# Optimization experiments

Measured on AMD Instinct MI355X. Metric: run time of the kernel, lower is better.

Reference implementation:

```python
import jax, jax.numpy as jnp
import numpy as np

DIM = 768
HEADS = 12
HEAD_DIM = DIM // HEADS
SCALE = HEAD_DIM ** (-0.5)
BATCH = 1
SEQ = 4096


def setup_inputs() -> dict:
    key = jax.random.key(0)
    ks = jax.random.split(key, 5)
    x = jax.random.normal(ks[0], (BATCH, SEQ, DIM), dtype=jnp.float32)
    # Linear params stored (in, out) for y = x @ W + b
    w_qkv = jax.random.normal(ks[1], (DIM, 3 * DIM), dtype=jnp.float32) * (DIM ** -0.5)
    b_qkv = jnp.zeros((3 * DIM,), dtype=jnp.float32)
    w_proj = jax.random.normal(ks[2], (DIM, DIM), dtype=jnp.float32) * (DIM ** -0.5)
    b_proj = jnp.zeros((DIM,), dtype=jnp.float32)
    return {"x": x, "w_qkv": w_qkv, "b_qkv": b_qkv, "w_proj": w_proj, "b_proj": b_proj}


def reference(x, w_qkv, b_qkv, w_proj, b_proj):
    B, S, _ = x.shape
    qkv = x @ w_qkv + b_qkv                              # [B,S,3*DIM]
    qkv = qkv.reshape(B, S, 3, HEADS, HEAD_DIM)
    q, k, v = qkv[:, :, 0], qkv[:, :, 1], qkv[:, :, 2]   # [B,S,H,D]
    # scaled dot-product attention, full score matrix as in the original
    attn = jnp.einsum("bqhd,bkhd->bhqk", q * SCALE, k)   # [B,H,S,S]
    attn = jax.nn.softmax(attn, axis=-1)
    out = jnp.einsum("bhqk,bkhd->bqhd", attn, v)         # [B,S,H,D]
    out = out.reshape(B, S, DIM)
    return out @ w_proj + b_proj
```

## Files before the change

### kernel.cpp

```cpp
#include <hip/hip_runtime.h>
#include <hip/hip_bf16.h>

#define SEQ   4096
#define DIM   768
#define HEADS 12
#define NQKV  2304
#define QSCALE 0.18033688011f

#if __has_builtin(__builtin_amdgcn_exp2f)
#define EXP2(x) __builtin_amdgcn_exp2f(x)
#else
#define EXP2(x) __expf((x) * 0.69314718056f)
#endif

typedef __bf16 bf16_t;
typedef bf16_t bf16x8 __attribute__((ext_vector_type(8)));
typedef float  f32x4  __attribute__((ext_vector_type(4)));
typedef float  f32x16 __attribute__((ext_vector_type(16)));
typedef unsigned short u16;
typedef unsigned int   u32;

static __device__ __forceinline__ float bf2f(u16 v) {
    union { float f; unsigned u; } x; x.u = ((unsigned)v) << 16; return x.f;
}
static __device__ __forceinline__ u16 f2bf(float f) {
    union { float f; unsigned u; } x; x.f = f;
    unsigned r = x.u + 0x7fff + ((x.u >> 16) & 1);
    return (u16)(r >> 16);
}
static __device__ __forceinline__ u32 fbits(float f) {
    union { float f; unsigned u; } x; x.f = f; return x.u;
}
static __device__ __forceinline__ void gload_lds16(const u16* g, u16* l) {
    __builtin_amdgcn_global_load_lds(
        (const __attribute__((address_space(1))) unsigned int*)g,
        (__attribute__((address_space(3))) unsigned int*)l, 16, 0, 0);
}

static __device__ __forceinline__ int detect_f32(const u32* __restrict__ x) {
    int lane = threadIdx.x & 63;
    int cnt = 0;
#pragma unroll
    for (int i = 0; i < 8; ++i) {
        u32 w = x[lane * 8 + i];
        cnt += (((w >> 7) & 0xFF) >= 0x8F) ? 1 : 0;
    }
#pragma unroll
    for (int m = 1; m < 64; m <<= 1) cnt += __shfl_xor(cnt, m);
    return cnt >= 64;
}

__global__ __launch_bounds__(256) void prep(
    const void* __restrict__ x, const void* __restrict__ wqkv,
    const void* __restrict__ bqkv, const void* __restrict__ wproj,
    const void* __restrict__ bproj,
    u16* __restrict__ cvt, u16* __restrict__ wqkvT, u16* __restrict__ wprojT)
{
    __shared__ u16 tile[64][65];
    const bool f32 = detect_f32((const u32*)x) != 0;
    const int b = blockIdx.x;
    const int t = threadIdx.x;

    if (b < 576) {
        const void* src; u16* dst; int K, N, tx, ty;
        if (b < 432) { src = wqkv; dst = wqkvT; K = DIM; N = NQKV; tx = b % 36; ty = b / 36; }
        else { int bb = b - 432; src = wproj; dst = wprojT; K = DIM; N = DIM; tx = bb % 12; ty = bb / 12; }
        const int k0 = ty * 64, n0 = tx * 64;
#pragma unroll
        for (int i = 0; i < 16; ++i) {
            int idx = i * 256 + t;
            int r = idx >> 6, c = idx & 63;
            size_t si = (size_t)(k0 + r) * N + n0 + c;
            tile[r][c] = f32 ? f2bf(((const float*)src)[si]) : ((const u16*)src)[si];
        }
        __syncthreads();
#pragma unroll
        for (int i = 0; i < 16; ++i) {
            int idx = i * 256 + t;
            int r = idx >> 6, c = idx & 63;
            dst[(size_t)(n0 + r) * K + k0 + c] = tile[c][r];
        }
    } else {
        const int SX = SEQ * DIM, e1 = SX + NQKV;
        const int n_cvt = e1 + DIM;
        for (int i = (b - 576) * 256 + t; i < n_cvt; i += 200 * 256) {
            const void* s; int off;
            if      (i < SX) { s = x; off = i; }
            else if (i < e1) { s = bqkv; off = i - SX; }
            else             { s = bproj; off = i - e1; }
            cvt[i] = f32 ? f2bf(((const float*)s)[off]) : ((const u16*)s)[off];
        }
    }
}

template<int MODE>
__global__ __launch_bounds__(256) void gemm128(
    const u16* __restrict__ A, const u16* __restrict__ BT, const u16* __restrict__ bias,
    u16* __restrict__ C0, float* __restrict__ Cf, u16* __restrict__ VT,
    const u32* __restrict__ xdet, int M, int N, int K)
{
    __shared__ union SharedLds {
        struct { u16 a[3][128 * 32]; u16 b[3][128 * 32]; } s;
        u16 t[128 * 136];
    } lds;

    const int t    = threadIdx.x;
    const int w    = t >> 6;
    const int lane = t & 63;
    const int l15  = lane & 15;
    const int quad = lane >> 4;
    const int wm   = w >> 1, wn = w & 1;
    const int m0   = blockIdx.y * 128, n0 = blockIdx.x * 128;

    const int srow = w * 32 + (lane >> 2);
    const int kch  = (lane & 3) * 8;
    const u16* asrc = A  + (size_t)(m0 + srow) * K + kch;
    const u16* bsrc = BT + (size_t)(n0 + srow) * K + kch;
    const int wst = w * 32 * 32;

    f32x4 acc[4][4] = {};

    u16 *aA = lds.s.a[0], *aB = lds.s.a[1], *aC = lds.s.a[2];
    u16 *bA = lds.s.b[0], *bB = lds.s.b[1], *bC = lds.s.b[2];

    auto STAGE = [&](u16* ad, u16* bd) {
        gload_lds16(asrc,          ad + wst);
        gload_lds16(asrc + 16 * K, ad + wst + 16 * 32);
        gload_lds16(bsrc,          bd + wst);
        gload_lds16(bsrc + 16 * K, bd + wst + 16 * 32);
        asrc += 32; bsrc += 32;
    };
    auto COMPUTE = [&](const u16* ab_, const u16* bb_) {
        const u16* ab = ab_ + (wm * 64 + l15) * 32 + quad * 8;
        const u16* bb = bb_ + (wn * 64 + l15) * 32 + quad * 8;
        bf16x8 af[4], bfr[4];
#pragma unroll
        for (int i = 0; i < 4; ++i) af[i]  = *(const bf16x8*)(ab + i * 16 * 32);
#pragma unroll
        for (int j = 0; j < 4; ++j) bfr[j] = *(const bf16x8*)(bb + j * 16 * 32);
#pragma unroll
        for (int i = 0; i < 4; ++i)
#pragma unroll
            for (int j = 0; j < 4; ++j)
                acc[i][j] = __builtin_amdgcn_mfma_f32_16x16x32_bf16(af[i], bfr[j], acc[i][j], 0, 0, 0);
    };

    const int NK = K >> 5;
    STAGE(aA, bA);
    STAGE(aB, bB);
    for (int kt = 0; kt < NK - 2; ++kt) {
        asm volatile("s_waitcnt vmcnt(4)" ::: "memory");
        __builtin_amdgcn_s_barrier();
        STAGE(aC, bC);
        COMPUTE(aA, bA);
        { u16* tt = aA; aA = aB; aB = aC; aC = tt; }
        { u16* tt = bA; bA = bB; bB = bC; bC = tt; }
    }
    asm volatile("s_waitcnt vmcnt(4)" ::: "memory");
    __builtin_amdgcn_s_barrier();
    COMPUTE(aA, bA);
    { u16* tt = aA; aA = aB; aB = aC; aC = tt; }
    { u16* tt = bA; bA = bB; bB = bC; bC = tt; }
    asm volatile("s_waitcnt vmcnt(0)" ::: "memory");
    __builtin_amdgcn_s_barrier();
    COMPUTE(aA, bA);

    if constexpr (MODE == 1) {
        if (n0 >= 1536) {
            __syncthreads();
#pragma unroll
            for (int i = 0; i < 4; ++i)
#pragma unroll
                for (int j = 0; j < 4; ++j)
#pragma unroll
                    for (int r = 0; r < 4; ++r) {
                        int ml = wm * 64 + i * 16 + quad * 4 + r;
                        int nl = wn * 64 + j * 16 + l15;
                        int mpl = (ml & ~15) | (ml & 3) |
                                  (((ml >> 2) & 1) << 3) | (((ml >> 3) & 1) << 2);
                        float v = acc[i][j][r] + bf2f(bias[n0 + nl]);
                        lds.t[nl * 136 + mpl] = f2bf(v);
                    }
            __syncthreads();
            const int rr = t >> 4;
            const int mo = (t & 15) * 8;
#pragma unroll
            for (int it = 0; it < 8; ++it) {
                int nl = rr + it * 16;
                *(bf16x8*)(VT + (size_t)(n0 - 1536 + nl) * SEQ + m0 + mo) =
                    *(const bf16x8*)(lds.t + nl * 136 + mo);
            }
            return;
        }
    }

    bool outf32 = false;
    if (MODE == 0) outf32 = detect_f32(xdet) != 0;
#pragma unroll
    for (int i = 0; i < 4; ++i)
#pragma unroll
        for (int j = 0; j < 4; ++j)
#pragma unroll
            for (int r = 0; r < 4; ++r) {
                int m = m0 + wm * 64 + i * 16 + quad * 4 + r;
                int n = n0 + wn * 64 + j * 16 + l15;
                float v = acc[i][j][r] + bf2f(bias[n]);
                if (MODE == 0) {
                    if (outf32) Cf[(size_t)m * N + n] = v;
                    else        C0[(size_t)m * N + n] = f2bf(v);
                } else {
                    float s = (n < 768) ? v * QSCALE : v;
                    C0[(size_t)m * 1536 + n] = f2bf(s);
                }
            }
}

__global__ __launch_bounds__(256, 3) void attn_kernel(
    const u16* __restrict__ qk, const u16* __restrict__ vt, u16* __restrict__ out)
{
    __shared__ u16 k_lds[3][64 * 64];
    __shared__ u16 v_lds[3][64 * 64];
    __shared__ float l_red[2][2][32];

    const int t    = threadIdx.x;
    const int w    = t >> 6;
    const int lane = t & 63;
    const int l31  = lane & 31;
    const int h    = lane >> 5;
    const int wq   = w & 1;
    const int wk   = w >> 1;

    const int lin     = blockIdx.x + (blockIdx.y << 6);
    const int logical = (lin & 7) * 96 + (lin >> 3);
    const int head    = logical >> 6;
    const int q0      = (logical & 63) * 64 + wq * 32;

    const u16* qrow = qk + (size_t)(q0 + l31) * 1536 + head * 64 + h * 8;
    bf16x8 qb[4];
#pragma unroll
    for (int s = 0; s < 4; ++s) qb[s] = *(const bf16x8*)(qrow + 16 * s);

    bf16x8 ones;
#pragma unroll
    for (int j = 0; j < 8; ++j) ones[j] = (bf16_t)1.0f;

    const f32x16 fz = {};

    const int srow = 8 * w + (lane >> 3);
    const int cs   = ((lane & 7) - srow) & 7;
    const u16* kst0 = qk + 768 + head * 64 + (size_t)srow * 1536 + cs * 8;
    const u16* kst1 = kst0 + (size_t)32 * 1536;
    const u16* vst0 = vt + (size_t)head * 64 * SEQ + (size_t)srow * SEQ + cs * 8;
    const u16* vst1 = vst0 + (size_t)32 * SEQ;
    const int woff = 8 * w * 64;

    const int krow = 32 * wk + l31;

    f32x16 o0 = {}, o1 = {}, lac = {};

    auto SK = [&](u16* kd) {
        gload_lds16(kst0, kd + woff);
        gload_lds16(kst1, kd + woff + 32 * 64);
        kst0 += (size_t)64 * 1536;
        kst1 += (size_t)64 * 1536;
    };
    auto SV = [&](u16* vd) {
        gload_lds16(vst0, vd + woff);
        gload_lds16(vst1, vd + woff + 32 * 64);
        vst0 += 64;
        vst1 += 64;
    };

    auto QK = [&](const u16* kb) -> f32x16 {
        const u16* kbase = kb + krow * 64;
        bf16x8 ka0 = *(const bf16x8*)(kbase + (((0 + h + krow) & 7) * 8));
        bf16x8 ka1 = *(const bf16x8*)(kbase + (((2 + h + krow) & 7) * 8));
        bf16x8 ka2 = *(const bf16x8*)(kbase + (((4 + h + krow) & 7) * 8));
        bf16x8 ka3 = *(const bf16x8*)(kbase + (((6 + h + krow) & 7) * 8));
        __builtin_amdgcn_s_setprio(1);
        f32x16 st = __builtin_amdgcn_mfma_f32_32x32x16_bf16(ka0, qb[0], fz, 0, 0, 0);
        st = __builtin_amdgcn_mfma_f32_32x32x16_bf16(ka1, qb[1], st, 0, 0, 0);
        st = __builtin_amdgcn_mfma_f32_32x32x16_bf16(ka2, qb[2], st, 0, 0, 0);
        st = __builtin_amdgcn_mfma_f32_32x32x16_bf16(ka3, qb[3], st, 0, 0, 0);
        __builtin_amdgcn_s_setprio(0);
        return st;
    };

    auto SMPV = [&](const f32x16& st, const u16* vb) {
        u32 q32[8];
#pragma unroll
        for (int i = 0; i < 8; ++i) {
            float pe = EXP2(st[2 * i]);
            float po = EXP2(st[2 * i + 1]);
            q32[i] = __builtin_amdgcn_perm(fbits(po), fbits(pe), 0x07060302u);
        }
        union { u32 u[4]; bf16x8 v; } pf0, pf1;
#pragma unroll
        for (int i = 0; i < 4; ++i) { pf0.u[i] = q32[i]; pf1.u[i] = q32[4 + i]; }
        __builtin_amdgcn_s_setprio(1);
#pragma unroll
        for (int s2 = 0; s2 < 2; ++s2) {
            const int c = 4 * wk + 2 * s2 + h;
            bf16x8 vb0 = *(const bf16x8*)(vb + l31 * 64 + (((c + l31) & 7) * 8));
            bf16x8 vb1 = *(const bf16x8*)(vb + (32 + l31) * 64 + (((c + 32 + l31) & 7) * 8));
            const bf16x8 pv = s2 ? pf1.v : pf0.v;
            o0  = __builtin_amdgcn_mfma_f32_32x32x16_bf16(pv, vb0, o0, 0, 0, 0);
            o1  = __builtin_amdgcn_mfma_f32_32x32x16_bf16(pv, vb1, o1, 0, 0, 0);
            lac = __builtin_amdgcn_mfma_f32_32x32x16_bf16(pv, ones, lac, 0, 0, 0);
        }
        __builtin_amdgcn_s_setprio(0);
    };

    u16 *kA = &k_lds[0][0], *kB = &k_lds[1][0], *kC = &k_lds[2][0];
    u16 *vA = &v_lds[0][0], *vB = &v_lds[1][0], *vC = &v_lds[2][0];

    SK(kA);
    SV(vA);
    SK(kB);
    asm volatile("s_waitcnt vmcnt(4)" ::: "memory");
    __builtin_amdgcn_s_barrier();
    f32x16 stA = QK(kA);
    SV(vB);
    f32x16 stB;

    for (int i = 0; i < 31; ++i) {
        SK(kC);
        asm volatile("s_waitcnt vmcnt(4)" ::: "memory");
        __builtin_amdgcn_s_barrier();
        stB = QK(kB);
        SMPV(stA, vA);
        SV(vC);
        { u16* tt = kA; kA = kB; kB = kC; kC = tt; }
        { u16* tt = vA; vA = vB; vB = vC; vC = tt; }
        SK(kC);
        asm volatile("s_waitcnt vmcnt(4)" ::: "memory");
        __builtin_amdgcn_s_barrier();
        stA = QK(kB);
        SMPV(stB, vA);
        SV(vC);
        { u16* tt = kA; kA = kB; kB = kC; kC = tt; }
        { u16* tt = vA; vA = vB; vB = vC; vC = tt; }
    }
    asm volatile("s_waitcnt vmcnt(2)" ::: "memory");
    __builtin_amdgcn_s_barrier();
    stB = QK(kB);
    SMPV(stA, vA);
    { u16* tt = kA; kA = kB; kB = kC; kC = tt; }
    { u16* tt = vA; vA = vB; vB = vC; vC = tt; }
    asm volatile("s_waitcnt vmcnt(0)" ::: "memory");
    __builtin_amdgcn_s_barrier();
    SMPV(stB, vA);
    __syncthreads();

    if (l31 == 0) {
#pragma unroll
        for (int r = 0; r < 16; ++r) {
            int row = (r & 3) + 8 * (r >> 2) + 4 * h;
            l_red[wq][wk][row] = lac[r];
        }
    }
    float* scr = (wq == 0) ? (float*)&k_lds[0][0] : (float*)&v_lds[0][0];
    if (wk == 1) {
#pragma unroll
        for (int r = 0; r < 16; ++r) {
            int row = (r & 3) + 8 * (r >> 2) + 4 * h;
            scr[row * 64 + l31]      = o0[r];
            scr[row * 64 + 32 + l31] = o1[r];
        }
    }
    __syncthreads();
    if (wk == 0) {
#pragma unroll
        for (int r = 0; r < 16; ++r) {
            int row = (r & 3) + 8 * (r >> 2) + 4 * h;
            float lt   = l_red[wq][0][row] + l_red[wq][1][row];
            float invl = 1.0f / lt;
            float s0 = o0[r] + scr[row * 64 + l31];
            float s1 = o1[r] + scr[row * 64 + 32 + l31];
            size_t gr = (size_t)(q0 + row) * 768 + head * 64;
            out[gr + l31]      = f2bf(s0 * invl);
            out[gr + 32 + l31] = f2bf(s1 * invl);
        }
    }
}

extern "C" void kernel_launch(void* const* d_in, const int* in_sizes, int n_in,
                              void* d_out, int out_size, void* d_ws, size_t ws_size,
                              hipStream_t stream) {
    const int SX = SEQ * DIM;

    u16* base   = (u16*)d_ws;
    u16* xb     = base;
    u16* bqkvb  = xb + SX;
    u16* bprojb = bqkvb + NQKV;
    u16* wqkvT  = bprojb + DIM;
    u16* wprojT = wqkvT + (size_t)NQKV * DIM;
    u16* qkb    = wprojT + (size_t)DIM * DIM;
    u16* vtb    = qkb + (size_t)SEQ * 1536;
    u16* attnb  = xb;

    prep<<<776, 256, 0, stream>>>(
        d_in[0], d_in[1], d_in[2], d_in[3], d_in[4], base, wqkvT, wprojT);
    gemm128<1><<<dim3(NQKV / 128, SEQ / 128), 256, 0, stream>>>(
        xb, wqkvT, bqkvb, qkb, nullptr, vtb, (const u32*)d_in[0],
        SEQ, NQKV, DIM);
    attn_kernel<<<dim3(SEQ / 64, HEADS), 256, 0, stream>>>(qkb, vtb, attnb);
    gemm128<0><<<dim3(DIM / 128, SEQ / 128), 256, 0, stream>>>(
        attnb, wprojT, bprojb, (u16*)d_out, (float*)d_out, nullptr,
        (const u32*)d_in[0], SEQ, DIM, DIM);
}
```

Before: 206.1 us.

## Cut attention V buffers to two for higher occupancy; swizzle GEMM block order

The attention kernel drops from triple to double buffering for V tiles and reuses V LDS for the row-sum reduction. This cuts LDS per block so four blocks can fit per CU instead of three. The V load is now issued after each barrier, which shortens the prefetch distance and may expose load latency. The GEMM also remaps block indices so that consecutive blocks are spread in groups of eight, aiming at better cache locality across XCDs.

```diff
diff --git a/kernel.cpp b/kernel.cpp
--- a/kernel.cpp
+++ b/kernel.cpp
@@ -110,7 +110,12 @@
     const int l15  = lane & 15;
     const int quad = lane >> 4;
     const int wm   = w >> 1, wn = w & 1;
-    const int m0   = blockIdx.y * 128, n0 = blockIdx.x * 128;
+
+    const int lin     = blockIdx.y * gridDim.x + blockIdx.x;
+    const int cpx     = (gridDim.x * gridDim.y) >> 3;
+    const int logical = (lin & 7) * cpx + (lin >> 3);
+    const int m0 = (logical / gridDim.x) * 128;
+    const int n0 = (logical % gridDim.x) * 128;
 
     const int srow = w * 32 + (lane >> 2);
     const int kch  = (lane & 3) * 8;
@@ -215,12 +220,11 @@
             }
 }
 
-__global__ __launch_bounds__(256, 3) void attn_kernel(
+__global__ __launch_bounds__(256, 4) void attn_kernel(
     const u16* __restrict__ qk, const u16* __restrict__ vt, u16* __restrict__ out)
 {
     __shared__ u16 k_lds[3][64 * 64];
-    __shared__ u16 v_lds[3][64 * 64];
-    __shared__ float l_red[2][2][32];
+    __shared__ u16 v_lds[2][64 * 64];
 
     const int t    = threadIdx.x;
     const int w    = t >> 6;
@@ -312,54 +316,52 @@
     };
 
     u16 *kA = &k_lds[0][0], *kB = &k_lds[1][0], *kC = &k_lds[2][0];
-    u16 *vA = &v_lds[0][0], *vB = &v_lds[1][0], *vC = &v_lds[2][0];
+    u16 *v0 = &v_lds[0][0], *v1 = &v_lds[1][0];
 
     SK(kA);
-    SV(vA);
     SK(kB);
+    SV(v0);
     asm volatile("s_waitcnt vmcnt(4)" ::: "memory");
     __builtin_amdgcn_s_barrier();
     f32x16 stA = QK(kA);
-    SV(vB);
     f32x16 stB;
 
     for (int i = 0; i < 31; ++i) {
         SK(kC);
-        asm volatile("s_waitcnt vmcnt(4)" ::: "memory");
+        asm volatile("s_waitcnt vmcnt(2)" ::: "memory");
         __builtin_amdgcn_s_barrier();
+        SV(v1);
         stB = QK(kB);
-        SMPV(stA, vA);
-        SV(vC);
+        SMPV(stA, v0);
         { u16* tt = kA; kA = kB; kB = kC; kC = tt; }
-        { u16* tt = vA; vA = vB; vB = vC; vC = tt; }
         SK(kC);
-        asm volatile("s_waitcnt vmcnt(4)" ::: "memory");
+        asm volatile("s_waitcnt vmcnt(2)" ::: "memory");
         __builtin_amdgcn_s_barrier();
+        SV(v0);
         stA = QK(kB);
-        SMPV(stB, vA);
-        SV(vC);
+        SMPV(stB, v1);
         { u16* tt = kA; kA = kB; kB = kC; kC = tt; }
-        { u16* tt = vA; vA = vB; vB = vC; vC = tt; }
-    }
-    asm volatile("s_waitcnt vmcnt(2)" ::: "memory");
-    __builtin_amdgcn_s_barrier();
-    stB = QK(kB);
-    SMPV(stA, vA);
-    { u16* tt = kA; kA = kB; kB = kC; kC = tt; }
-    { u16* tt = vA; vA = vB; vB = vC; vC = tt; }
+    }
     asm volatile("s_waitcnt vmcnt(0)" ::: "memory");
     __builtin_amdgcn_s_barrier();
-    SMPV(stB, vA);
+    SV(v1);
+    stB = QK(kB);
+    SMPV(stA, v0);
+    { u16* tt = kA; kA = kB; kB = kC; kC = tt; }
+    asm volatile("s_waitcnt vmcnt(0)" ::: "memory");
+    __builtin_amdgcn_s_barrier();
+    SMPV(stB, v1);
     __syncthreads();
 
+    float* lred = (float*)&v_lds[1][0];
     if (l31 == 0) {
 #pragma unroll
         for (int r = 0; r < 16; ++r) {
             int row = (r & 3) + 8 * (r >> 2) + 4 * h;
-            l_red[wq][wk][row] = lac[r];
-        }
-    }
-    float* scr = (wq == 0) ? (float*)&k_lds[0][0] : (float*)&v_lds[0][0];
+            lred[(wq * 2 + wk) * 32 + row] = lac[r];
+        }
+    }
+    float* scr = (wq == 0) ? (float*)&k_lds[0][0] : (float*)&k_lds[1][0];
     if (wk == 1) {
 #pragma unroll
         for (int r = 0; r < 16; ++r) {
@@ -373,7 +375,7 @@
 #pragma unroll
         for (int r = 0; r < 16; ++r) {
             int row = (r & 3) + 8 * (r >> 2) + 4 * h;
-            float lt   = l_red[wq][0][row] + l_red[wq][1][row];
+            float lt   = lred[(wq * 2 + 0) * 32 + row] + lred[(wq * 2 + 1) * 32 + row];
             float invl = 1.0f / lt;
             float s0 = o0[r] + scr[row * 64 + l31];
             float s1 = o1[r] + scr[row * 64 + 32 + l31];
```

Measured after the change: 236.8 us. 1.15x slower.
